# Kernel optimization log

Measured on AMD Instinct MI355X. Metric: run time of the kernel, lower is better.

## Reference

```python
import jax, jax.numpy as jnp
import numpy as np

N_NODES = 10000
N_EDGES = 160000
C = 128           # channel multiplicity
D_DOWN = 64       # node_feats_down '64x0e'
D_RAD = 8         # radial basis size
AVG_NEIGH = 16.0
INV_SQRT3 = 1.0 / np.sqrt(3.0)  # CG coeff for 1o x 1o -> 0e


def setup_inputs() -> dict:
    key = jax.random.key(0)
    ks = jax.random.split(key, 20)
    inp = {
        "node_attrs": jax.random.normal(ks[0], (N_NODES, 10), jnp.float32),
        "node_feats": jax.random.normal(ks[1], (N_NODES, 4 * C), jnp.float32),
        "edge_attrs": jax.random.normal(ks[2], (N_EDGES, 4), jnp.float32),
        "edge_feats": jax.random.uniform(ks[3], (N_EDGES, D_RAD), jnp.float32),
        "edge_index": jax.random.randint(ks[4], (N_EDGES, 2), 0, N_NODES, jnp.int32),
        # linear_up: 128x0e+128x1o -> 128x0e+128x1o (per-irrep channel mixing)
        "W_up0": jax.random.normal(ks[5], (C, C), jnp.float32),
        "W_up1": jax.random.normal(ks[6], (C, C), jnp.float32),
        # linear_down: 128x0e+128x1o -> 64x0e (only scalars map)
        "W_down": jax.random.normal(ks[7], (C, D_DOWN), jnp.float32),
        # radial MLP [136, 256, 256, 256, 512]
        "Wm0": jax.random.normal(ks[8], (D_RAD + 2 * D_DOWN, 256), jnp.float32),
        "Wm1": jax.random.normal(ks[9], (256, 256), jnp.float32),
        "Wm2": jax.random.normal(ks[10], (256, 256), jnp.float32),
        "Wm3": jax.random.normal(ks[11], (256, 4 * C), jnp.float32),
        # linear: irreps_mid (2x128x0e + 2x128x1o) -> 128x0e+128x1o
        "W_lin0": jax.random.normal(ks[12], (2 * C, C), jnp.float32),
        "W_lin1": jax.random.normal(ks[13], (2 * C, C), jnp.float32),
        # skip_linear: 128x0e+128x1o -> 128x0e+128x1o
        "W_skip0": jax.random.normal(ks[14], (C, C), jnp.float32),
        "W_skip1": jax.random.normal(ks[15], (C, C), jnp.float32),
    }
    return inp


def _split(x):
    # [N, 512] -> scalars [N,128], vectors [N,128,3]
    return x[:, :C], x[:, C:].reshape(-1, C, 3)


def _irrep_linear(s, v, W0, W1):
    # e3nn Linear with 1/sqrt(fan_in) normalization, per-irrep
    a = (s @ W0) / np.sqrt(C)
    b = jnp.einsum("nic,ij->njc", v, W1) / np.sqrt(C)
    return a, b


def reference(node_attrs, node_feats, edge_attrs, edge_feats, edge_index,
              W_up0, W_up1, W_down, Wm0, Wm1, Wm2, Wm3,
              W_lin0, W_lin1, W_skip0, W_skip1):
    n_nodes = node_feats.shape[0]
    sender = edge_index[:, 0]
    receiver = edge_index[:, 1]

    s, v = _split(node_feats)

    # skip connection
    sc_s, sc_v = _irrep_linear(s, v, W_skip0, W_skip1)
    sc = jnp.concatenate([sc_s, sc_v.reshape(n_nodes, 3 * C)], axis=-1)

    # linear_up / linear_down
    up_s, up_v = _irrep_linear(s, v, W_up0, W_up1)
    down = (s @ W_down) / np.sqrt(C)  # [N, 64]

    # radial MLP on augmented edge feats
    aug = jnp.concatenate([edge_feats, down[sender], down[receiver]], axis=-1)  # [E,136]
    h = jax.nn.silu((aug @ Wm0) / np.sqrt(aug.shape[-1]))
    h = jax.nn.silu((h @ Wm1) / np.sqrt(256.0))
    h = jax.nn.silu((h @ Wm2) / np.sqrt(256.0))
    tpw = (h @ Wm3) / np.sqrt(256.0)  # [E, 512]
    w1, w2, w3, w4 = tpw[:, :C], tpw[:, C:2*C], tpw[:, 2*C:3*C], tpw[:, 3*C:]

    # per-edge CG tensor product (uvu, external weights)
    xs = up_s[sender]           # [E,128] gathered 0e
    xv = up_v[sender]           # [E,128,3] gathered 1o
    y0 = edge_attrs[:, :1]      # [E,1]   sh 0e
    yv = edge_attrs[:, 1:4]     # [E,3]   sh 1o

    out0a = w1 * xs * y0                                       # 0e x 0e -> 0e
    out0b = w4 * jnp.einsum("eic,ec->ei", xv, yv) * INV_SQRT3  # 1o x 1o -> 0e
    out1a = (w2 * xs)[:, :, None] * yv[:, None, :]             # 0e x 1o -> 1o
    out1b = w3[:, :, None] * xv * y0[:, :, None]               # 1o x 0e -> 1o

    mid0 = jnp.concatenate([out0a, out0b], axis=-1)  # [E,256]
    mid1 = jnp.concatenate([out1a, out1b], axis=1)   # [E,256,3]

    # scatter-sum messages to receivers
    m0 = jax.ops.segment_sum(mid0, receiver, num_segments=n_nodes)
    m1 = jax.ops.segment_sum(mid1, receiver, num_segments=n_nodes)

    # final per-irrep linear, divided by avg_num_neighbors
    msg_s = (m0 @ W_lin0) / np.sqrt(2.0 * C) / AVG_NEIGH                       # [N,128]
    msg_v = jnp.einsum("nic,ij->njc", m1, W_lin1) / np.sqrt(2.0 * C) / AVG_NEIGH  # [N,128,3]

    # reshape_irreps: [N, channels, 1+3]
    out = jnp.concatenate([msg_s[:, :, None], msg_v], axis=-1)  # [N,128,4]
    return out, sc
```

## Files before the change

### kernel.cpp

```cpp
#include <hip/hip_runtime.h>
#include <cmath>

#define NN 10000
#define NE 160000
#define INV_SQRT_C 0.08838834764831845f
#define INV_SQRT3F 0.5773502691896258f

typedef _Float16 f16x8 __attribute__((ext_vector_type(8)));
typedef _Float16 f16x4 __attribute__((ext_vector_type(4)));
typedef _Float16 f16x2 __attribute__((ext_vector_type(2)));
typedef float    f32x4 __attribute__((ext_vector_type(4)));

__device__ __forceinline__ float silu_f(float x) {
  return x / (1.f + __expf(-x));
}

__global__ void wconv(const float* __restrict__ src, _Float16* __restrict__ dst,
                      int Korig, int Kpad, int N, float scale, int P) {
  int total = Kpad * N;
  for (int t = blockIdx.x * blockDim.x + threadIdx.x; t < total;
       t += gridDim.x * blockDim.x) {
    int n = t % N;
    int k = t / N;
    int kb = k >> 5, kk = k & 31;
    int sub = n & (P - 1);
    int n_l = (n & ~(P - 1)) | ((sub & 15) * (P >> 4) + (sub >> 4));
    float v = (k < Korig) ? src[(size_t)k * N + n_l] * scale : 0.f;
    dst[((size_t)(kb * N + n) << 5) + kk] = (_Float16)v;
  }
}

__global__ __launch_bounds__(256) void node_pre_s(
    const float* __restrict__ feats,
    const float* __restrict__ W_up0, const float* __restrict__ W_skip0,
    const float* __restrict__ W_down,
    _Float16* __restrict__ UPH, _Float16* __restrict__ DOWNH,
    float* __restrict__ out_sc) {
  __shared__ float ls[16 * 128];
  const int n0 = blockIdx.x * 16;
  const int t = threadIdx.x;
  for (int f = t; f < 16 * 128; f += 256) {
    int r = f >> 7, c = f & 127;
    ls[r * 128 + c] = feats[(size_t)(n0 + r) * 512 + c];
  }
  __syncthreads();
  {
    int j = t & 127, g = t >> 7;
    float au[8] = {0, 0, 0, 0, 0, 0, 0, 0};
    float ak[8] = {0, 0, 0, 0, 0, 0, 0, 0};
    for (int i = 0; i < 128; ++i) {
      float wu = W_up0[(size_t)i * 128 + j];
      float wk = W_skip0[(size_t)i * 128 + j];
#pragma unroll
      for (int r = 0; r < 8; ++r) {
        float s = ls[(g * 8 + r) * 128 + i];
        au[r] += s * wu;
        ak[r] += s * wk;
      }
    }
#pragma unroll
    for (int r = 0; r < 8; ++r) {
      int n = n0 + g * 8 + r;
      UPH[(size_t)n * 512 + j] = (_Float16)(au[r] * INV_SQRT_C);
      out_sc[(size_t)n * 512 + j] = ak[r] * INV_SQRT_C;
    }
  }
  {
    int j = t & 63, g = t >> 6;
    float ad[4] = {0, 0, 0, 0};
    for (int i = 0; i < 128; ++i) {
      float wd = W_down[(size_t)i * 64 + j];
#pragma unroll
      for (int r = 0; r < 4; ++r) ad[r] += ls[(g * 4 + r) * 128 + i] * wd;
    }
#pragma unroll
    for (int r = 0; r < 4; ++r)
      DOWNH[(size_t)(n0 + g * 4 + r) * 64 + j] = (_Float16)(ad[r] * INV_SQRT_C);
  }
}

__global__ __launch_bounds__(256) void node_pre_v(
    const float* __restrict__ feats,
    const float* __restrict__ W_up1, const float* __restrict__ W_skip1,
    _Float16* __restrict__ UPH, float* __restrict__ out_sc) {
  __shared__ float ls[16 * 384];
  const int n0 = blockIdx.x * 16;
  const int t = threadIdx.x;
  for (int f = t; f < 16 * 384; f += 256) {
    int r = f / 384, c = f % 384;
    ls[r * 384 + c] = feats[(size_t)(n0 + r) * 512 + 128 + c];
  }
  __syncthreads();
  int j = t & 127, g = t >> 7;
  float au[8][3], ak[8][3];
#pragma unroll
  for (int r = 0; r < 8; ++r)
#pragma unroll
    for (int c = 0; c < 3; ++c) { au[r][c] = 0.f; ak[r][c] = 0.f; }
  for (int i = 0; i < 128; ++i) {
    float wu = W_up1[(size_t)i * 128 + j];
    float wk = W_skip1[(size_t)i * 128 + j];
#pragma unroll
    for (int r = 0; r < 8; ++r) {
#pragma unroll
      for (int c = 0; c < 3; ++c) {
        float v = ls[(g * 8 + r) * 384 + i * 3 + c];
        au[r][c] += v * wu;
        ak[r][c] += v * wk;
      }
    }
  }
#pragma unroll
  for (int r = 0; r < 8; ++r) {
    int n = n0 + g * 8 + r;
#pragma unroll
    for (int c = 0; c < 3; ++c) {
      UPH[(size_t)n * 512 + 128 + j * 3 + c] = (_Float16)(au[r][c] * INV_SQRT_C);
      out_sc[(size_t)n * 512 + 128 + j * 3 + c] = ak[r][c] * INV_SQRT_C;
    }
  }
}

__global__ void k_count(const int* __restrict__ edge_index, int* __restrict__ CNT,
                        int col) {
  int e = blockIdx.x * blockDim.x + threadIdx.x;
  if (e < NE) atomicAdd(&CNT[edge_index[e * 2 + col]], 1);
}

__global__ __launch_bounds__(1024) void k_scan(const int* __restrict__ CNT,
                                               int* __restrict__ OFF,
                                               int* __restrict__ CUR) {
  __shared__ int ts[1024];
  const int t = threadIdx.x;
  const int base = t * 10;
  int loc[10];
  int s = 0;
#pragma unroll
  for (int i = 0; i < 10; ++i) {
    int idx = base + i;
    int v = (idx < NN) ? CNT[idx] : 0;
    loc[i] = s;
    s += v;
  }
  ts[t] = s;
  __syncthreads();
  for (int off = 1; off < 1024; off <<= 1) {
    int v = (t >= off) ? ts[t - off] : 0;
    __syncthreads();
    ts[t] += v;
    __syncthreads();
  }
  int tp = (t > 0) ? ts[t - 1] : 0;
#pragma unroll
  for (int i = 0; i < 10; ++i) {
    int idx = base + i;
    if (idx < NN) {
      OFF[idx] = tp + loc[i];
      CUR[idx] = tp + loc[i];
    }
  }
  if (t == 1023) OFF[NN] = ts[1023];
}

__global__ void k_fill(const int* __restrict__ edge_index, int* __restrict__ CUR,
                       int* __restrict__ IDX, int col) {
  int e = blockIdx.x * blockDim.x + threadIdx.x;
  if (e < NE) {
    int r = edge_index[e * 2 + col];
    int pos = atomicAdd(&CUR[r], 1);
    IDX[pos] = e;
  }
}

__device__ __forceinline__ void mlp_layer_256(
    const _Float16* In, _Float16* Out, const _Float16* __restrict__ Wz,
    int m, int g, int wv) {
  f32x4 acc[4][4];
  f32x4 zero4 = {0.f, 0.f, 0.f, 0.f};
#pragma unroll
  for (int rt = 0; rt < 4; ++rt)
#pragma unroll
    for (int ct = 0; ct < 4; ++ct) acc[rt][ct] = zero4;

#pragma unroll
  for (int kb = 0; kb < 8; ++kb) {
    f16x8 a[4], b[4];
#pragma unroll
    for (int rt = 0; rt < 4; ++rt) {
      int row = rt * 16 + m;
      a[rt] = *(const f16x8*)&In[row * 256 + (((kb * 2 + (g >> 1)) ^ m) << 4) + (g & 1) * 8];
    }
#pragma unroll
    for (int ct = 0; ct < 4; ++ct)
      b[ct] = *(const f16x8*)&Wz[((size_t)(kb * 256 + wv * 64 + ct * 16 + m) << 5) + g * 8];
#pragma unroll
    for (int rt = 0; rt < 4; ++rt)
#pragma unroll
      for (int ct = 0; ct < 4; ++ct)
        acc[rt][ct] = __builtin_amdgcn_mfma_f32_16x16x32_f16(a[rt], b[ct], acc[rt][ct], 0, 0, 0);
  }
#pragma unroll
  for (int rt = 0; rt < 4; ++rt)
#pragma unroll
    for (int q = 0; q < 4; ++q) {
      int row = rt * 16 + g * 4 + q;
      f16x4 pk;
#pragma unroll
      for (int ct = 0; ct < 4; ++ct) pk[ct] = (_Float16)silu_f(acc[rt][ct][q]);
      int blk = (wv * 4 + (m >> 2)) ^ (row & 15);
      *(f16x4*)&Out[row * 256 + (blk << 4) + (m & 3) * 4] = pk;
    }
}

__global__ __launch_bounds__(256, 2) void edge_mlp(
    const float* __restrict__ edge_attrs,
    const float* __restrict__ edge_feats,
    const int* __restrict__ edge_index,
    const int* __restrict__ SIDX,
    const _Float16* __restrict__ DOWNH,
    const _Float16* __restrict__ UPH,
    const _Float16* __restrict__ W0h, const _Float16* __restrict__ W1h,
    const _Float16* __restrict__ W2h, const _Float16* __restrict__ W3h,
    const _Float16* __restrict__ WL0h, const _Float16* __restrict__ WL1h,
    _Float16* __restrict__ MIDs) {
  __shared__ _Float16 HA[64 * 256];
  __shared__ _Float16 HB[64 * 256];

  const int tid = threadIdx.x;
  const int lane = tid & 63;
  const int wv = tid >> 6;
  const int m = lane & 15;
  const int g = lane >> 4;
  const int e0 = blockIdx.x * 64;
  const int nw = wv * 64;

  int el_r[4], snd_r[4], rcv_r[4];
#pragma unroll
  for (int rt = 0; rt < 4; ++rt) {
    el_r[rt] = SIDX[e0 + rt * 16 + m];
    int2 sr = *(const int2*)&edge_index[(size_t)el_r[rt] * 2];
    snd_r[rt] = sr.x;
    rcv_r[rt] = sr.y;
  }

  f32x4 zero4 = {0.f, 0.f, 0.f, 0.f};
  f16x8 zf = {0, 0, 0, 0, 0, 0, 0, 0};

  {
    f32x4 acc[4][4];
#pragma unroll
    for (int rt = 0; rt < 4; ++rt)
#pragma unroll
      for (int ct = 0; ct < 4; ++ct) acc[rt][ct] = zero4;

#pragma unroll
    for (int kb = 0; kb < 5; ++kb) {
      const int k0 = kb * 32 + g * 8;
      f16x8 a[4], b[4];
#pragma unroll
      for (int rt = 0; rt < 4; ++rt) {
        if (k0 == 0) {
          const float* ef = &edge_feats[(size_t)el_r[rt] * 8];
          float4 f0 = *(const float4*)ef;
          float4 f1 = *(const float4*)(ef + 4);
          f16x8 av;
          av[0] = (_Float16)f0.x; av[1] = (_Float16)f0.y;
          av[2] = (_Float16)f0.z; av[3] = (_Float16)f0.w;
          av[4] = (_Float16)f1.x; av[5] = (_Float16)f1.y;
          av[6] = (_Float16)f1.z; av[7] = (_Float16)f1.w;
          a[rt] = av;
        } else if (k0 < 72) {
          a[rt] = *(const f16x8*)&DOWNH[(size_t)snd_r[rt] * 64 + (k0 - 8)];
        } else if (k0 < 136) {
          a[rt] = *(const f16x8*)&DOWNH[(size_t)rcv_r[rt] * 64 + (k0 - 72)];
        } else {
          a[rt] = zf;
        }
      }
#pragma unroll
      for (int ct = 0; ct < 4; ++ct)
        b[ct] = *(const f16x8*)&W0h[((size_t)(kb * 256 + nw + ct * 16 + m) << 5) + g * 8];
#pragma unroll
      for (int rt = 0; rt < 4; ++rt)
#pragma unroll
        for (int ct = 0; ct < 4; ++ct)
          acc[rt][ct] = __builtin_amdgcn_mfma_f32_16x16x32_f16(a[rt], b[ct], acc[rt][ct], 0, 0, 0);
    }
#pragma unroll
    for (int rt = 0; rt < 4; ++rt)
#pragma unroll
      for (int q = 0; q < 4; ++q) {
        int row = rt * 16 + g * 4 + q;
        f16x4 pk;
#pragma unroll
        for (int ct = 0; ct < 4; ++ct) pk[ct] = (_Float16)silu_f(acc[rt][ct][q]);
        int blk = (wv * 4 + (m >> 2)) ^ (row & 15);
        *(f16x4*)&HA[row * 256 + (blk << 4) + (m & 3) * 4] = pk;
      }
  }
  __syncthreads();

  mlp_layer_256(HA, HB, W1h, m, g, wv);
  __syncthreads();
  mlp_layer_256(HB, HA, W2h, m, g, wv);
  __syncthreads();

  _Float16* SW = HB;
  _Float16* SP = HB + 64 * 128;

  const int e_loc = lane;
  const int ers = (e_loc ^ (e_loc >> 3)) & 7;
  const int elc = SIDX[e0 + e_loc];
  const int snd_e = edge_index[(size_t)elc * 2];
  const _Float16* uprow = &UPH[(size_t)snd_e * 512];

  auto qgemm = [&](int qbase, f32x4 (&accq)[4][2]) {
#pragma unroll
    for (int rt = 0; rt < 4; ++rt)
#pragma unroll
      for (int ct = 0; ct < 2; ++ct) accq[rt][ct] = zero4;
#pragma unroll
    for (int kb = 0; kb < 8; ++kb) {
      f16x8 a[4], b[2];
#pragma unroll
      for (int rt = 0; rt < 4; ++rt) {
        int row = rt * 16 + m;
        a[rt] = *(const f16x8*)&HA[row * 256 + (((kb * 2 + (g >> 1)) ^ m) << 4) + (g & 1) * 8];
      }
#pragma unroll
      for (int ct = 0; ct < 2; ++ct)
        b[ct] = *(const f16x8*)&W3h[((size_t)(kb * 512 + qbase + wv * 32 + ct * 16 + m) << 5) + g * 8];
#pragma unroll
      for (int rt = 0; rt < 4; ++rt)
#pragma unroll
        for (int ct = 0; ct < 2; ++ct)
          accq[rt][ct] = __builtin_amdgcn_mfma_f32_16x16x32_f16(a[rt], b[ct], accq[rt][ct], 0, 0, 0);
    }
  };

  auto sw_write = [&](const f32x4 (&accq)[4][2]) {
#pragma unroll
    for (int rt = 0; rt < 4; ++rt)
#pragma unroll
      for (int r4 = 0; r4 < 4; ++r4) {
        int row = rt * 16 + g * 4 + r4;
        int rs = (row ^ (row >> 3)) & 7;
        f16x2 pk;
        pk[0] = (_Float16)accq[rt][0][r4];
        pk[1] = (_Float16)accq[rt][1][r4];
        int blk = ((wv * 2 + (m >> 3)) ^ rs) & 7;
        *(f16x2*)&SW[row * 128 + (blk << 4) + (m & 7) * 2] = pk;
      }
  };

  auto fold = [&](const _Float16* __restrict__ WLh, int qpart, f32x4 (&P)[4][2]) {
#pragma unroll
    for (int rt = 0; rt < 4; ++rt)
#pragma unroll
      for (int ct = 0; ct < 2; ++ct) P[rt][ct] = zero4;
#pragma unroll
    for (int kb = 0; kb < 4; ++kb) {
      f16x8 a[4], b[2];
#pragma unroll
      for (int rt = 0; rt < 4; ++rt) {
        int row = rt * 16 + m;
        int rs = (row ^ (row >> 3)) & 7;
        a[rt] = *(const f16x8*)&SP[row * 128 + ((((kb * 2 + (g >> 1)) ^ rs) & 7) << 4) + (g & 1) * 8];
      }
#pragma unroll
      for (int ct = 0; ct < 2; ++ct)
        b[ct] = *(const f16x8*)&WLh[((size_t)((qpart * 4 + kb) * 128 + wv * 32 + ct * 16 + m) << 5) + g * 8];
#pragma unroll
      for (int rt = 0; rt < 4; ++rt)
#pragma unroll
        for (int ct = 0; ct < 2; ++ct)
          P[rt][ct] = __builtin_amdgcn_mfma_f32_16x16x32_f16(a[rt], b[ct], P[rt][ct], 0, 0, 0);
    }
  };

  auto tp_xs = [&]() {
#pragma unroll
    for (int cch = 0; cch < 4; ++cch) {
      int ib = nw / 2 + cch * 8;
      int blk = ((ib >> 4) ^ ers) & 7;
      int off = e_loc * 128 + (blk << 4) + (ib & 15);
      f16x8 swv = *(const f16x8*)&SW[off];
      f16x8 upv = *(const f16x8*)&uprow[ib];
      f16x8 pr = swv * upv;
      *(f16x8*)&SP[off] = pr;
    }
  };

  _Float16 xvb[96];
  auto load_xv = [&]() {
#pragma unroll
    for (int u = 0; u < 12; ++u) {
      f16x8 t = *(const f16x8*)&uprow[128 + wv * 96 + u * 8];
#pragma unroll
      for (int z = 0; z < 8; ++z) xvb[u * 8 + z] = t[z];
    }
  };

  auto tp_w4 = [&]() {
    float4 ea = *(const float4*)&edge_attrs[(size_t)elc * 4];
#pragma unroll
    for (int cch = 0; cch < 4; ++cch) {
      int ib = nw / 2 + cch * 8;
      int blk = ((ib >> 4) ^ ers) & 7;
      int off = e_loc * 128 + (blk << 4) + (ib & 15);
      f16x8 swv = *(const f16x8*)&SW[off];
      f16x8 outv;
#pragma unroll
      for (int z = 0; z < 8; ++z) {
        int k = cch * 8 + z;
        float d = (float)xvb[k * 3] * ea.y + (float)xvb[k * 3 + 1] * ea.z +
                  (float)xvb[k * 3 + 2] * ea.w;
        outv[z] = (_Float16)((float)swv[z] * d);
      }
      *(f16x8*)&SP[off] = outv;
    }
  };

  auto tp_w3 = [&](int c) {
#pragma unroll
    for (int cch = 0; cch < 4; ++cch) {
      int ib = nw / 2 + cch * 8;
      int blk = ((ib >> 4) ^ ers) & 7;
      int off = e_loc * 128 + (blk << 4) + (ib & 15);
      f16x8 swv = *(const f16x8*)&SW[off];
      f16x8 outv;
#pragma unroll
      for (int z = 0; z < 8; ++z) {
        int k = cch * 8 + z;
        outv[z] = swv[z] * xvb[k * 3 + c];
      }
      *(f16x8*)&SP[off] = outv;
    }
  };

  f32x4 accqA[4][2], accqB[4][2];
  f32x4 P1[4][2], P4[4][2], P2[4][2], P3[4][2];

  qgemm(0, accqA);
  sw_write(accqA);
  tp_xs();
  qgemm(384, accqB);
  __syncthreads();
  fold(WL0h, 0, P1);
  sw_write(accqB);
  load_xv();
  __syncthreads();
  tp_w4();
  qgemm(128, accqA);
  __syncthreads();
  fold(WL0h, 1, P4);
  sw_write(accqA);

#pragma unroll
  for (int rt = 0; rt < 4; ++rt)
#pragma unroll
    for (int r4 = 0; r4 < 4; ++r4) {
      int row = rt * 16 + g * 4 + r4;
      int elw = SIDX[e0 + row];
      float4 ea = *(const float4*)&edge_attrs[(size_t)elw * 4];
      f16x2 pk;
      pk[0] = (_Float16)(ea.x * P1[rt][0][r4] + INV_SQRT3F * P4[rt][0][r4]);
      pk[1] = (_Float16)(ea.x * P1[rt][1][r4] + INV_SQRT3F * P4[rt][1][r4]);
      *(f16x2*)&MIDs[(size_t)elw * 512 + wv * 32 + m * 2] = pk;
    }
  __syncthreads();
  tp_xs();
  qgemm(256, accqB);
  __syncthreads();
  fold(WL1h, 0, P2);
  sw_write(accqB);
  __syncthreads();

#pragma unroll
  for (int c = 0; c < 3; ++c) {
    tp_w3(c);
    __syncthreads();
    fold(WL1h, 1, P3);
#pragma unroll
    for (int rt = 0; rt < 4; ++rt)
#pragma unroll
      for (int r4 = 0; r4 < 4; ++r4) {
        int row = rt * 16 + g * 4 + r4;
        int elw = SIDX[e0 + row];
        float4 ea = *(const float4*)&edge_attrs[(size_t)elw * 4];
        float yvc = (c == 0) ? ea.y : (c == 1) ? ea.z : ea.w;
        f16x2 pk;
        pk[0] = (_Float16)(yvc * P2[rt][0][r4] + ea.x * P3[rt][0][r4]);
        pk[1] = (_Float16)(yvc * P2[rt][1][r4] + ea.x * P3[rt][1][r4]);
        *(f16x2*)&MIDs[(size_t)elw * 512 + 128 + c * 128 + wv * 32 + m * 2] = pk;
      }
    if (c < 2) __syncthreads();
  }
}

__global__ __launch_bounds__(256) void gather_msg(
    const _Float16* __restrict__ MIDs, const int* __restrict__ OFF,
    const int* __restrict__ EIDX, float* __restrict__ out) {
  __shared__ int eb[256];
  __shared__ float os[512];
  const int n = blockIdx.x;
  const int t = threadIdx.x;
  const int beg = OFF[n], end = OFF[n + 1];
  float a0 = 0.f, a1 = 0.f;
  for (int base = beg; base < end; base += 256) {
    int cnt = min(256, end - base);
    __syncthreads();
    if (t < cnt) eb[t] = EIDX[base + t];
    __syncthreads();
    int k = 0;
    for (; k + 4 <= cnt; k += 4) {
      int e0_ = eb[k], e1_ = eb[k + 1], e2_ = eb[k + 2], e3_ = eb[k + 3];
      f16x2 v0 = *(const f16x2*)&MIDs[(size_t)e0_ * 512 + t * 2];
      f16x2 v1 = *(const f16x2*)&MIDs[(size_t)e1_ * 512 + t * 2];
      f16x2 v2 = *(const f16x2*)&MIDs[(size_t)e2_ * 512 + t * 2];
      f16x2 v3 = *(const f16x2*)&MIDs[(size_t)e3_ * 512 + t * 2];
      a0 += (float)v0[0] + (float)v1[0] + (float)v2[0] + (float)v3[0];
      a1 += (float)v0[1] + (float)v1[1] + (float)v2[1] + (float)v3[1];
    }
    for (; k < cnt; ++k) {
      f16x2 v = *(const f16x2*)&MIDs[(size_t)eb[k] * 512 + t * 2];
      a0 += (float)v[0];
      a1 += (float)v[1];
    }
  }
#pragma unroll
  for (int u = 0; u < 2; ++u) {
    int x = t * 2 + u;
    float a = u ? a1 : a0;
    int dst;
    if (x < 128) {
      dst = x * 4;
    } else {
      int xm = x - 128;
      int c = xm >> 7, j = xm & 127;
      dst = j * 4 + 1 + c;
    }
    os[dst] = a;
  }
  __syncthreads();
  *(float2*)&out[(size_t)n * 512 + t * 2] = *(const float2*)&os[t * 2];
}

extern "C" void kernel_launch(void* const* d_in, const int* in_sizes, int n_in,
                              void* d_out, int out_size, void* d_ws, size_t ws_size,
                              hipStream_t stream) {
  const float* node_feats = (const float*)d_in[1];
  const float* edge_attrs = (const float*)d_in[2];
  const float* edge_feats = (const float*)d_in[3];
  const int*   edge_index = (const int*)d_in[4];
  const float* W_up0   = (const float*)d_in[5];
  const float* W_up1   = (const float*)d_in[6];
  const float* W_down  = (const float*)d_in[7];
  const float* Wm0     = (const float*)d_in[8];
  const float* Wm1     = (const float*)d_in[9];
  const float* Wm2     = (const float*)d_in[10];
  const float* Wm3     = (const float*)d_in[11];
  const float* W_lin0  = (const float*)d_in[12];
  const float* W_lin1  = (const float*)d_in[13];
  const float* W_skip0 = (const float*)d_in[14];
  const float* W_skip1 = (const float*)d_in[15];
  float* out = (float*)d_out;

  char* ws = (char*)d_ws;
  size_t off = 0;
  auto alloc = [&](size_t bytes) {
    void* p = ws + off;
    off = (off + bytes + 255) & ~(size_t)255;
    return p;
  };
  _Float16* UPH   = (_Float16*)alloc((size_t)NN * 512 * 2);
  _Float16* DOWNH = (_Float16*)alloc((size_t)NN * 64 * 2);
  _Float16* W0h   = (_Float16*)alloc(160 * 256 * 2);
  _Float16* W1h   = (_Float16*)alloc(256 * 256 * 2);
  _Float16* W2h   = (_Float16*)alloc(256 * 256 * 2);
  _Float16* W3h   = (_Float16*)alloc(256 * 512 * 2);
  _Float16* WL0h  = (_Float16*)alloc(256 * 128 * 2);
  _Float16* WL1h  = (_Float16*)alloc(256 * 128 * 2);
  int*      CNT   = (int*)alloc((size_t)NN * 4);
  int*      OFF   = (int*)alloc((size_t)(NN + 1) * 4);
  int*      CUR   = (int*)alloc((size_t)NN * 4);
  int*      EIDX  = (int*)alloc((size_t)NE * 4);
  int*      CNT2  = (int*)alloc((size_t)NN * 4);
  int*      OFF2  = (int*)alloc((size_t)(NN + 1) * 4);
  int*      CUR2  = (int*)alloc((size_t)NN * 4);
  int*      SIDX  = (int*)alloc((size_t)NE * 4);
  _Float16* MIDs  = (_Float16*)alloc((size_t)NE * 512 * 2);

  hipMemsetAsync(CNT, 0, (size_t)NN * 4, stream);
  hipMemsetAsync(CNT2, 0, (size_t)NN * 4, stream);

  wconv<<<160, 256, 0, stream>>>(Wm0, W0h, 136, 160, 256, 1.0f / sqrtf(136.0f), 64);
  wconv<<<256, 256, 0, stream>>>(Wm1, W1h, 256, 256, 256, 0.0625f, 64);
  wconv<<<256, 256, 0, stream>>>(Wm2, W2h, 256, 256, 256, 0.0625f, 64);
  wconv<<<512, 256, 0, stream>>>(Wm3, W3h, 256, 256, 512, 0.0625f, 32);
  wconv<<<128, 256, 0, stream>>>(W_lin0, WL0h, 256, 256, 128, 1.0f / 256.0f, 32);
  wconv<<<128, 256, 0, stream>>>(W_lin1, WL1h, 256, 256, 128, 1.0f / 256.0f, 32);

  node_pre_s<<<625, 256, 0, stream>>>(node_feats, W_up0, W_skip0, W_down,
                                      UPH, DOWNH, out + (size_t)NN * 512);
  node_pre_v<<<625, 256, 0, stream>>>(node_feats, W_up1, W_skip1,
                                      UPH, out + (size_t)NN * 512);

  k_count<<<625, 256, 0, stream>>>(edge_index, CNT, 1);
  k_count<<<625, 256, 0, stream>>>(edge_index, CNT2, 0);
  k_scan<<<1, 1024, 0, stream>>>(CNT, OFF, CUR);
  k_scan<<<1, 1024, 0, stream>>>(CNT2, OFF2, CUR2);
  k_fill<<<625, 256, 0, stream>>>(edge_index, CUR, EIDX, 1);
  k_fill<<<625, 256, 0, stream>>>(edge_index, CUR2, SIDX, 0);

  edge_mlp<<<2500, 256, 0, stream>>>(edge_attrs, edge_feats, edge_index, SIDX,
                                     DOWNH, UPH, W0h, W1h, W2h, W3h, WL0h, WL1h,
                                     MIDs);
  gather_msg<<<NN, 256, 0, stream>>>(MIDs, OFF, EIDX, out);
}
```

Baseline: 520.3 us.

## Shrink edge MLP shared memory with in-place layers to fit three blocks per CU

```diff
diff --git a/kernel.cpp b/kernel.cpp
--- a/kernel.cpp
+++ b/kernel.cpp
@@ -172,8 +172,8 @@
   }
 }
 
-__device__ __forceinline__ void mlp_layer_256(
-    const _Float16* In, _Float16* Out, const _Float16* __restrict__ Wz,
+__device__ __forceinline__ void mlp_layer_ip(
+    _Float16* Buf, const _Float16* __restrict__ Wz,
     int m, int g, int wv) {
   f32x4 acc[4][4];
   f32x4 zero4 = {0.f, 0.f, 0.f, 0.f};
@@ -188,7 +188,7 @@
 #pragma unroll
     for (int rt = 0; rt < 4; ++rt) {
       int row = rt * 16 + m;
-      a[rt] = *(const f16x8*)&In[row * 256 + (((kb * 2 + (g >> 1)) ^ m) << 4) + (g & 1) * 8];
+      a[rt] = *(const f16x8*)&Buf[row * 256 + (((kb * 2 + (g >> 1)) ^ m) << 4) + (g & 1) * 8];
     }
 #pragma unroll
     for (int ct = 0; ct < 4; ++ct)
@@ -199,6 +199,7 @@
       for (int ct = 0; ct < 4; ++ct)
         acc[rt][ct] = __builtin_amdgcn_mfma_f32_16x16x32_f16(a[rt], b[ct], acc[rt][ct], 0, 0, 0);
   }
+  __syncthreads();
 #pragma unroll
   for (int rt = 0; rt < 4; ++rt)
 #pragma unroll
@@ -208,11 +209,11 @@
 #pragma unroll
       for (int ct = 0; ct < 4; ++ct) pk[ct] = (_Float16)silu_f(acc[rt][ct][q]);
       int blk = (wv * 4 + (m >> 2)) ^ (row & 15);
-      *(f16x4*)&Out[row * 256 + (blk << 4) + (m & 3) * 4] = pk;
-    }
-}
-
-__global__ __launch_bounds__(256, 2) void edge_mlp(
+      *(f16x4*)&Buf[row * 256 + (blk << 4) + (m & 3) * 4] = pk;
+    }
+}
+
+__global__ __launch_bounds__(256, 3) void edge_mlp(
     const float* __restrict__ edge_attrs,
     const float* __restrict__ edge_feats,
     const int* __restrict__ edge_index,
@@ -224,7 +225,9 @@
     const _Float16* __restrict__ WL0h, const _Float16* __restrict__ WL1h,
     _Float16* __restrict__ MIDs) {
   __shared__ _Float16 HA[64 * 256];
-  __shared__ _Float16 HB[64 * 256];
+  __shared__ _Float16 SWP[64 * 128];
+  __shared__ int    SIDs[64];
+  __shared__ float4 EAs[64];
 
   const int tid = threadIdx.x;
   const int lane = tid & 63;
@@ -233,6 +236,12 @@
   const int g = lane >> 4;
   const int e0 = blockIdx.x * 64;
   const int nw = wv * 64;
+
+  if (tid < 64) {
+    int el = SIDX[e0 + tid];
+    SIDs[tid] = el;
+    EAs[tid] = *(const float4*)&edge_attrs[(size_t)el * 4];
+  }
 
   int el_r[4], snd_r[4], rcv_r[4];
 #pragma unroll
@@ -300,17 +309,14 @@
   }
   __syncthreads();
 
-  mlp_layer_256(HA, HB, W1h, m, g, wv);
-  __syncthreads();
-  mlp_layer_256(HB, HA, W2h, m, g, wv);
-  __syncthreads();
-
-  _Float16* SW = HB;
-  _Float16* SP = HB + 64 * 128;
+  mlp_layer_ip(HA, W1h, m, g, wv);
+  __syncthreads();
+  mlp_layer_ip(HA, W2h, m, g, wv);
+  __syncthreads();
 
   const int e_loc = lane;
   const int ers = (e_loc ^ (e_loc >> 3)) & 7;
-  const int elc = SIDX[e0 + e_loc];
+  const int elc = SIDs[e_loc];
   const int snd_e = edge_index[(size_t)elc * 2];
   const _Float16* uprow = &UPH[(size_t)snd_e * 512];
 
@@ -349,7 +355,7 @@
         pk[0] = (_Float16)accq[rt][0][r4];
         pk[1] = (_Float16)accq[rt][1][r4];
         int blk = ((wv * 2 + (m >> 3)) ^ rs) & 7;
-        *(f16x2*)&SW[row * 128 + (blk << 4) + (m & 7) * 2] = pk;
+        *(f16x2*)&SWP[row * 128 + (blk << 4) + (m & 7) * 2] = pk;
       }
   };
 
@@ -365,7 +371,7 @@
       for (int rt = 0; rt < 4; ++rt) {
         int row = rt * 16 + m;
         int rs = (row ^ (row >> 3)) & 7;
-        a[rt] = *(const f16x8*)&SP[row * 128 + ((((kb * 2 + (g >> 1)) ^ rs) & 7) << 4) + (g & 1) * 8];
+        a[rt] = *(const f16x8*)&SWP[row * 128 + ((((kb * 2 + (g >> 1)) ^ rs) & 7) << 4) + (g & 1) * 8];
       }
 #pragma unroll
       for (int ct = 0; ct < 2; ++ct)
@@ -384,10 +390,10 @@
       int ib = nw / 2 + cch * 8;
       int blk = ((ib >> 4) ^ ers) & 7;
       int off = e_loc * 128 + (blk << 4) + (ib & 15);
-      f16x8 swv = *(const f16x8*)&SW[off];
+      f16x8 swv = *(const f16x8*)&SWP[off];
       f16x8 upv = *(const f16x8*)&uprow[ib];
       f16x8 pr = swv * upv;
-      *(f16x8*)&SP[off] = pr;
+      *(f16x8*)&SWP[off] = pr;
     }
   };
 
@@ -402,13 +408,13 @@
   };
 
   auto tp_w4 = [&]() {
-    float4 ea = *(const float4*)&edge_attrs[(size_t)elc * 4];
+    float4 ea = EAs[e_loc];
 #pragma unroll
     for (int cch = 0; cch < 4; ++cch) {
       int ib = nw / 2 + cch * 8;
       int blk = ((ib >> 4) ^ ers) & 7;
       int off = e_loc * 128 + (blk << 4) + (ib & 15);
-      f16x8 swv = *(const f16x8*)&SW[off];
+      f16x8 swv = *(const f16x8*)&SWP[off];
       f16x8 outv;
 #pragma unroll
       for (int z = 0; z < 8; ++z) {
@@ -417,68 +423,69 @@
                   (float)xvb[k * 3 + 2] * ea.w;
         outv[z] = (_Float16)((float)swv[z] * d);
       }
-      *(f16x8*)&SP[off] = outv;
+      *(f16x8*)&SWP[off] = outv;
     }
   };
 
-  auto tp_w3 = [&](int c) {
+  f32x4 accqA[4][2], accqB[4][2];
+  f32x4 P1[4][2], P4[4][2], P2[4][2], P3[4][2];
+
+  qgemm(0, accqA);
+  sw_write(accqA);
+  tp_xs();
+  qgemm(384, accqB);
+  __syncthreads();
+  fold(WL0h, 0, P1);
+  load_xv();
+  __syncthreads();
+  sw_write(accqB);
+  tp_w4();
+  qgemm(128, accqA);
+  __syncthreads();
+  fold(WL0h, 1, P4);
+  __syncthreads();
+  sw_write(accqA);
+  tp_xs();
+  qgemm(256, accqB);
+
+#pragma unroll
+  for (int rt = 0; rt < 4; ++rt)
+#pragma unroll
+    for (int r4 = 0; r4 < 4; ++r4) {
+      int row = rt * 16 + g * 4 + r4;
+      int elw = SIDs[row];
+      float4 ea = EAs[row];
+      f16x2 pk;
+      pk[0] = (_Float16)(ea.x * P1[rt][0][r4] + INV_SQRT3F * P4[rt][0][r4]);
+      pk[1] = (_Float16)(ea.x * P1[rt][1][r4] + INV_SQRT3F * P4[rt][1][r4]);
+      *(f16x2*)&MIDs[(size_t)elw * 512 + wv * 32 + m * 2] = pk;
+    }
+  __syncthreads();
+  fold(WL1h, 0, P2);
+  __syncthreads();
+  sw_write(accqB);
+
+  f16x8 w3r[4];
+#pragma unroll
+  for (int cch = 0; cch < 4; ++cch) {
+    int ib = nw / 2 + cch * 8;
+    int blk = ((ib >> 4) ^ ers) & 7;
+    w3r[cch] = *(const f16x8*)&SWP[e_loc * 128 + (blk << 4) + (ib & 15)];
+  }
+
+#pragma unroll
+  for (int c = 0; c < 3; ++c) {
 #pragma unroll
     for (int cch = 0; cch < 4; ++cch) {
       int ib = nw / 2 + cch * 8;
       int blk = ((ib >> 4) ^ ers) & 7;
       int off = e_loc * 128 + (blk << 4) + (ib & 15);
-      f16x8 swv = *(const f16x8*)&SW[off];
       f16x8 outv;
 #pragma unroll
-      for (int z = 0; z < 8; ++z) {
-        int k = cch * 8 + z;
-        outv[z] = swv[z] * xvb[k * 3 + c];
-      }
-      *(f16x8*)&SP[off] = outv;
-    }
-  };
-
-  f32x4 accqA[4][2], accqB[4][2];
-  f32x4 P1[4][2], P4[4][2], P2[4][2], P3[4][2];
-
-  qgemm(0, accqA);
-  sw_write(accqA);
-  tp_xs();
-  qgemm(384, accqB);
-  __syncthreads();
-  fold(WL0h, 0, P1);
-  sw_write(accqB);
-  load_xv();
-  __syncthreads();
-  tp_w4();
-  qgemm(128, accqA);
-  __syncthreads();
-  fold(WL0h, 1, P4);
-  sw_write(accqA);
-
-#pragma unroll
-  for (int rt = 0; rt < 4; ++rt)
-#pragma unroll
-    for (int r4 = 0; r4 < 4; ++r4) {
-      int row = rt * 16 + g * 4 + r4;
-      int elw = SIDX[e0 + row];
-      float4 ea = *(const float4*)&edge_attrs[(size_t)elw * 4];
-      f16x2 pk;
-      pk[0] = (_Float16)(ea.x * P1[rt][0][r4] + INV_SQRT3F * P4[rt][0][r4]);
-      pk[1] = (_Float16)(ea.x * P1[rt][1][r4] + INV_SQRT3F * P4[rt][1][r4]);
-      *(f16x2*)&MIDs[(size_t)elw * 512 + wv * 32 + m * 2] = pk;
-    }
-  __syncthreads();
-  tp_xs();
-  qgemm(256, accqB);
-  __syncthreads();
-  fold(WL1h, 0, P2);
-  sw_write(accqB);
-  __syncthreads();
-
-#pragma unroll
-  for (int c = 0; c < 3; ++c) {
-    tp_w3(c);
+      for (int z = 0; z < 8; ++z)
+        outv[z] = w3r[cch][z] * xvb[(cch * 8 + z) * 3 + c];
+      *(f16x8*)&SWP[off] = outv;
+    }
     __syncthreads();
     fold(WL1h, 1, P3);
 #pragma unroll
@@ -486,8 +493,8 @@
 #pragma unroll
       for (int r4 = 0; r4 < 4; ++r4) {
         int row = rt * 16 + g * 4 + r4;
-        int elw = SIDX[e0 + row];
-        float4 ea = *(const float4*)&edge_attrs[(size_t)elw * 4];
+        int elw = SIDs[row];
+        float4 ea = EAs[row];
         float yvc = (c == 0) ? ea.y : (c == 1) ? ea.z : ea.w;
         f16x2 pk;
         pk[0] = (_Float16)(yvc * P2[rt][0][r4] + ea.x * P3[rt][0][r4]);
```

New measurement: 635.6 us. +22.2%, slower.

## Merge setup kernels into fewer launches and write MIDs in sender-sorted order

Applied to the files above, without the earlier changes.

```diff
diff --git a/kernel.cpp b/kernel.cpp
--- a/kernel.cpp
+++ b/kernel.cpp
@@ -15,8 +15,9 @@
   return x / (1.f + __expf(-x));
 }
 
-__global__ void wconv(const float* __restrict__ src, _Float16* __restrict__ dst,
-                      int Korig, int Kpad, int N, float scale, int P) {
+__device__ __forceinline__ void wconv_one(
+    const float* __restrict__ src, _Float16* __restrict__ dst,
+    int Korig, int Kpad, int N, float scale, int P) {
   int total = Kpad * N;
   for (int t = blockIdx.x * blockDim.x + threadIdx.x; t < total;
        t += gridDim.x * blockDim.x) {
@@ -30,107 +31,123 @@
   }
 }
 
-__global__ __launch_bounds__(256) void node_pre_s(
+__global__ __launch_bounds__(256) void wconv6(
+    const float* __restrict__ s0, const float* __restrict__ s1,
+    const float* __restrict__ s2, const float* __restrict__ s3,
+    const float* __restrict__ s4, const float* __restrict__ s5,
+    _Float16* __restrict__ d0, _Float16* __restrict__ d1,
+    _Float16* __restrict__ d2, _Float16* __restrict__ d3,
+    _Float16* __restrict__ d4, _Float16* __restrict__ d5) {
+  switch (blockIdx.y) {
+    case 0: wconv_one(s0, d0, 136, 160, 256, 0.08574929257125442f, 64); break;
+    case 1: wconv_one(s1, d1, 256, 256, 256, 0.0625f, 64); break;
+    case 2: wconv_one(s2, d2, 256, 256, 256, 0.0625f, 64); break;
+    case 3: wconv_one(s3, d3, 256, 256, 512, 0.0625f, 32); break;
+    case 4: wconv_one(s4, d4, 256, 256, 128, 1.0f / 256.0f, 32); break;
+    default: wconv_one(s5, d5, 256, 256, 128, 1.0f / 256.0f, 32); break;
+  }
+}
+
+__global__ __launch_bounds__(256) void node_pre_all(
     const float* __restrict__ feats,
     const float* __restrict__ W_up0, const float* __restrict__ W_skip0,
     const float* __restrict__ W_down,
+    const float* __restrict__ W_up1, const float* __restrict__ W_skip1,
     _Float16* __restrict__ UPH, _Float16* __restrict__ DOWNH,
     float* __restrict__ out_sc) {
-  __shared__ float ls[16 * 128];
-  const int n0 = blockIdx.x * 16;
+  __shared__ float ls[16 * 384];
   const int t = threadIdx.x;
-  for (int f = t; f < 16 * 128; f += 256) {
-    int r = f >> 7, c = f & 127;
-    ls[r * 128 + c] = feats[(size_t)(n0 + r) * 512 + c];
-  }
-  __syncthreads();
-  {
+  if (blockIdx.x < 625) {
+    const int n0 = blockIdx.x * 16;
+    for (int f = t; f < 16 * 128; f += 256) {
+      int r = f >> 7, c = f & 127;
+      ls[r * 128 + c] = feats[(size_t)(n0 + r) * 512 + c];
+    }
+    __syncthreads();
+    {
+      int j = t & 127, g = t >> 7;
+      float au[8] = {0, 0, 0, 0, 0, 0, 0, 0};
+      float ak[8] = {0, 0, 0, 0, 0, 0, 0, 0};
+      for (int i = 0; i < 128; ++i) {
+        float wu = W_up0[(size_t)i * 128 + j];
+        float wk = W_skip0[(size_t)i * 128 + j];
+#pragma unroll
+        for (int r = 0; r < 8; ++r) {
+          float s = ls[(g * 8 + r) * 128 + i];
+          au[r] += s * wu;
+          ak[r] += s * wk;
+        }
+      }
+#pragma unroll
+      for (int r = 0; r < 8; ++r) {
+        int n = n0 + g * 8 + r;
+        UPH[(size_t)n * 512 + j] = (_Float16)(au[r] * INV_SQRT_C);
+        out_sc[(size_t)n * 512 + j] = ak[r] * INV_SQRT_C;
+      }
+    }
+    {
+      int j = t & 63, g = t >> 6;
+      float ad[4] = {0, 0, 0, 0};
+      for (int i = 0; i < 128; ++i) {
+        float wd = W_down[(size_t)i * 64 + j];
+#pragma unroll
+        for (int r = 0; r < 4; ++r) ad[r] += ls[(g * 4 + r) * 128 + i] * wd;
+      }
+#pragma unroll
+      for (int r = 0; r < 4; ++r)
+        DOWNH[(size_t)(n0 + g * 4 + r) * 64 + j] = (_Float16)(ad[r] * INV_SQRT_C);
+    }
+  } else {
+    const int n0 = (blockIdx.x - 625) * 16;
+    for (int f = t; f < 16 * 384; f += 256) {
+      int r = f / 384, c = f % 384;
+      ls[r * 384 + c] = feats[(size_t)(n0 + r) * 512 + 128 + c];
+    }
+    __syncthreads();
     int j = t & 127, g = t >> 7;
-    float au[8] = {0, 0, 0, 0, 0, 0, 0, 0};
-    float ak[8] = {0, 0, 0, 0, 0, 0, 0, 0};
+    float au[8][3], ak[8][3];
+#pragma unroll
+    for (int r = 0; r < 8; ++r)
+#pragma unroll
+      for (int c = 0; c < 3; ++c) { au[r][c] = 0.f; ak[r][c] = 0.f; }
     for (int i = 0; i < 128; ++i) {
-      float wu = W_up0[(size_t)i * 128 + j];
-      float wk = W_skip0[(size_t)i * 128 + j];
+      float wu = W_up1[(size_t)i * 128 + j];
+      float wk = W_skip1[(size_t)i * 128 + j];
 #pragma unroll
       for (int r = 0; r < 8; ++r) {
-        float s = ls[(g * 8 + r) * 128 + i];
-        au[r] += s * wu;
-        ak[r] += s * wk;
+#pragma unroll
+        for (int c = 0; c < 3; ++c) {
+          float v = ls[(g * 8 + r) * 384 + i * 3 + c];
+          au[r][c] += v * wu;
+          ak[r][c] += v * wk;
+        }
       }
     }
 #pragma unroll
     for (int r = 0; r < 8; ++r) {
       int n = n0 + g * 8 + r;
-      UPH[(size_t)n * 512 + j] = (_Float16)(au[r] * INV_SQRT_C);
-      out_sc[(size_t)n * 512 + j] = ak[r] * INV_SQRT_C;
-    }
-  }
-  {
-    int j = t & 63, g = t >> 6;
-    float ad[4] = {0, 0, 0, 0};
-    for (int i = 0; i < 128; ++i) {
-      float wd = W_down[(size_t)i * 64 + j];
-#pragma unroll
-      for (int r = 0; r < 4; ++r) ad[r] += ls[(g * 4 + r) * 128 + i] * wd;
-    }
-#pragma unroll
-    for (int r = 0; r < 4; ++r)
-      DOWNH[(size_t)(n0 + g * 4 + r) * 64 + j] = (_Float16)(ad[r] * INV_SQRT_C);
-  }
-}
-
-__global__ __launch_bounds__(256) void node_pre_v(
-    const float* __restrict__ feats,
-    const float* __restrict__ W_up1, const float* __restrict__ W_skip1,
-    _Float16* __restrict__ UPH, float* __restrict__ out_sc) {
-  __shared__ float ls[16 * 384];
-  const int n0 = blockIdx.x * 16;
-  const int t = threadIdx.x;
-  for (int f = t; f < 16 * 384; f += 256) {
-    int r = f / 384, c = f % 384;
-    ls[r * 384 + c] = feats[(size_t)(n0 + r) * 512 + 128 + c];
-  }
-  __syncthreads();
-  int j = t & 127, g = t >> 7;
-  float au[8][3], ak[8][3];
-#pragma unroll
-  for (int r = 0; r < 8; ++r)
-#pragma unroll
-    for (int c = 0; c < 3; ++c) { au[r][c] = 0.f; ak[r][c] = 0.f; }
-  for (int i = 0; i < 128; ++i) {
-    float wu = W_up1[(size_t)i * 128 + j];
-    float wk = W_skip1[(size_t)i * 128 + j];
-#pragma unroll
-    for (int r = 0; r < 8; ++r) {
 #pragma unroll
       for (int c = 0; c < 3; ++c) {
-        float v = ls[(g * 8 + r) * 384 + i * 3 + c];
-        au[r][c] += v * wu;
-        ak[r][c] += v * wk;
-      }
-    }
-  }
-#pragma unroll
-  for (int r = 0; r < 8; ++r) {
-    int n = n0 + g * 8 + r;
-#pragma unroll
-    for (int c = 0; c < 3; ++c) {
-      UPH[(size_t)n * 512 + 128 + j * 3 + c] = (_Float16)(au[r][c] * INV_SQRT_C);
-      out_sc[(size_t)n * 512 + 128 + j * 3 + c] = ak[r][c] * INV_SQRT_C;
-    }
-  }
-}
-
-__global__ void k_count(const int* __restrict__ edge_index, int* __restrict__ CNT,
-                        int col) {
+        UPH[(size_t)n * 512 + 128 + j * 3 + c] = (_Float16)(au[r][c] * INV_SQRT_C);
+        out_sc[(size_t)n * 512 + 128 + j * 3 + c] = ak[r][c] * INV_SQRT_C;
+      }
+    }
+  }
+}
+
+__global__ void k_count2(const int* __restrict__ edge_index,
+                         int* __restrict__ CNT, int* __restrict__ CNT2) {
   int e = blockIdx.x * blockDim.x + threadIdx.x;
-  if (e < NE) atomicAdd(&CNT[edge_index[e * 2 + col]], 1);
-}
-
-__global__ __launch_bounds__(1024) void k_scan(const int* __restrict__ CNT,
-                                               int* __restrict__ OFF,
-                                               int* __restrict__ CUR) {
-  __shared__ int ts[1024];
+  if (e < NE) {
+    int2 sr = *(const int2*)&edge_index[(size_t)e * 2];
+    atomicAdd(&CNT[sr.y], 1);
+    atomicAdd(&CNT2[sr.x], 1);
+  }
+}
+
+__device__ __forceinline__ void scan_one(const int* __restrict__ CNT,
+                                         int* __restrict__ OFF,
+                                         int* __restrict__ CUR, int* ts) {
   const int t = threadIdx.x;
   const int base = t * 10;
   int loc[10];
@@ -162,13 +179,24 @@
   if (t == 1023) OFF[NN] = ts[1023];
 }
 
-__global__ void k_fill(const int* __restrict__ edge_index, int* __restrict__ CUR,
-                       int* __restrict__ IDX, int col) {
+__global__ __launch_bounds__(1024) void k_scan2(
+    const int* __restrict__ CNT, int* __restrict__ OFF, int* __restrict__ CUR,
+    const int* __restrict__ CNT2, int* __restrict__ OFF2, int* __restrict__ CUR2) {
+  __shared__ int ts[1024];
+  if (blockIdx.x == 0) scan_one(CNT, OFF, CUR, ts);
+  else                 scan_one(CNT2, OFF2, CUR2, ts);
+}
+
+__global__ void k_fill2(const int* __restrict__ edge_index,
+                        int* __restrict__ CUR, int* __restrict__ EIDX,
+                        int* __restrict__ CUR2, int* __restrict__ SIDX) {
   int e = blockIdx.x * blockDim.x + threadIdx.x;
   if (e < NE) {
-    int r = edge_index[e * 2 + col];
-    int pos = atomicAdd(&CUR[r], 1);
-    IDX[pos] = e;
+    int2 sr = *(const int2*)&edge_index[(size_t)e * 2];
+    int ps = atomicAdd(&CUR2[sr.x], 1);
+    SIDX[ps] = e;
+    int pr = atomicAdd(&CUR[sr.y], 1);
+    EIDX[pr] = ps;
   }
 }
 
@@ -466,7 +494,7 @@
       f16x2 pk;
       pk[0] = (_Float16)(ea.x * P1[rt][0][r4] + INV_SQRT3F * P4[rt][0][r4]);
       pk[1] = (_Float16)(ea.x * P1[rt][1][r4] + INV_SQRT3F * P4[rt][1][r4]);
-      *(f16x2*)&MIDs[(size_t)elw * 512 + wv * 32 + m * 2] = pk;
+      *(f16x2*)&MIDs[(size_t)(e0 + row) * 512 + wv * 32 + m * 2] = pk;
     }
   __syncthreads();
   tp_xs();
@@ -492,7 +520,7 @@
         f16x2 pk;
         pk[0] = (_Float16)(yvc * P2[rt][0][r4] + ea.x * P3[rt][0][r4]);
         pk[1] = (_Float16)(yvc * P2[rt][1][r4] + ea.x * P3[rt][1][r4]);
-        *(f16x2*)&MIDs[(size_t)elw * 512 + 128 + c * 128 + wv * 32 + m * 2] = pk;
+        *(f16x2*)&MIDs[(size_t)(e0 + row) * 512 + 128 + c * 128 + wv * 32 + m * 2] = pk;
       }
     if (c < 2) __syncthreads();
   }
@@ -581,37 +609,29 @@
   _Float16* W3h   = (_Float16*)alloc(256 * 512 * 2);
   _Float16* WL0h  = (_Float16*)alloc(256 * 128 * 2);
   _Float16* WL1h  = (_Float16*)alloc(256 * 128 * 2);
-  int*      CNT   = (int*)alloc((size_t)NN * 4);
+  int*      CNTS  = (int*)alloc((size_t)2 * NN * 4);
+  int*      CNT   = CNTS;
+  int*      CNT2  = CNTS + NN;
   int*      OFF   = (int*)alloc((size_t)(NN + 1) * 4);
   int*      CUR   = (int*)alloc((size_t)NN * 4);
   int*      EIDX  = (int*)alloc((size_t)NE * 4);
-  int*      CNT2  = (int*)alloc((size_t)NN * 4);
   int*      OFF2  = (int*)alloc((size_t)(NN + 1) * 4);
   int*      CUR2  = (int*)alloc((size_t)NN * 4);
   int*      SIDX  = (int*)alloc((size_t)NE * 4);
   _Float16* MIDs  = (_Float16*)alloc((size_t)NE * 512 * 2);
 
-  hipMemsetAsync(CNT, 0, (size_t)NN * 4, stream);
-  hipMemsetAsync(CNT2, 0, (size_t)NN * 4, stream);
-
-  wconv<<<160, 256, 0, stream>>>(Wm0, W0h, 136, 160, 256, 1.0f / sqrtf(136.0f), 64);
-  wconv<<<256, 256, 0, stream>>>(Wm1, W1h, 256, 256, 256, 0.0625f, 64);
-  wconv<<<256, 256, 0, stream>>>(Wm2, W2h, 256, 256, 256, 0.0625f, 64);
-  wconv<<<512, 256, 0, stream>>>(Wm3, W3h, 256, 256, 512, 0.0625f, 32);
-  wconv<<<128, 256, 0, stream>>>(W_lin0, WL0h, 256, 256, 128, 1.0f / 256.0f, 32);
-  wconv<<<128, 256, 0, stream>>>(W_lin1, WL1h, 256, 256, 128, 1.0f / 256.0f, 32);
-
-  node_pre_s<<<625, 256, 0, stream>>>(node_feats, W_up0, W_skip0, W_down,
-                                      UPH, DOWNH, out + (size_t)NN * 512);
-  node_pre_v<<<625, 256, 0, stream>>>(node_feats, W_up1, W_skip1,
-                                      UPH, out + (size_t)NN * 512);
-
-  k_count<<<625, 256, 0, stream>>>(edge_index, CNT, 1);
-  k_count<<<625, 256, 0, stream>>>(edge_index, CNT2, 0);
-  k_scan<<<1, 1024, 0, stream>>>(CNT, OFF, CUR);
-  k_scan<<<1, 1024, 0, stream>>>(CNT2, OFF2, CUR2);
-  k_fill<<<625, 256, 0, stream>>>(edge_index, CUR, EIDX, 1);
-  k_fill<<<625, 256, 0, stream>>>(edge_index, CUR2, SIDX, 0);
+  hipMemsetAsync(CNTS, 0, (size_t)2 * NN * 4, stream);
+
+  wconv6<<<dim3(128, 6), 256, 0, stream>>>(Wm0, Wm1, Wm2, Wm3, W_lin0, W_lin1,
+                                           W0h, W1h, W2h, W3h, WL0h, WL1h);
+
+  node_pre_all<<<1250, 256, 0, stream>>>(node_feats, W_up0, W_skip0, W_down,
+                                         W_up1, W_skip1,
+                                         UPH, DOWNH, out + (size_t)NN * 512);
+
+  k_count2<<<625, 256, 0, stream>>>(edge_index, CNT, CNT2);
+  k_scan2<<<2, 1024, 0, stream>>>(CNT, OFF, CUR, CNT2, OFF2, CUR2);
+  k_fill2<<<625, 256, 0, stream>>>(edge_index, CUR, EIDX, CUR2, SIDX);
 
   edge_mlp<<<2500, 256, 0, stream>>>(edge_attrs, edge_feats, edge_index, SIDX,
                                      DOWNH, UPH, W0h, W1h, W2h, W3h, WL0h, WL1h,
```

New measurement: 474.0 us. -8.9%, faster.
